# Optimization experiments

Measured on AMD Instinct MI355X. Metric: run time of the kernel, lower is better.

Reference implementation:

```python
import jax, jax.numpy as jnp
import numpy as np

BIG = 1e10  # sentinel for invalid pairwise distances


def get_xyz(depth, fx, fy, cx, cy):
    # depth: [B,1,H,W] -> xyz: [B,3,H,W] via pinhole unprojection
    B, _, H, W = depth.shape
    v = jnp.arange(H, dtype=depth.dtype)[:, None]   # rows
    u = jnp.arange(W, dtype=depth.dtype)[None, :]   # cols
    z = depth[:, 0]                                  # [B,H,W]
    x = (u - cx) / fx * z
    y = (v - cy) / fy * z
    return jnp.stack([x, y, z], axis=1)              # [B,3,H,W]


def _chamfer_item(p, g, vp, vg):
    # p,g: [N,3] point sets; vp,vg: [N] bool validity masks
    # squared pairwise distances via ||p||^2 + ||g||^2 - 2 p.g
    d = (jnp.sum(p * p, -1)[:, None] + jnp.sum(g * g, -1)[None, :]
         - 2.0 * (p @ g.T))                          # [N,N]
    d = jnp.maximum(d, 0.0)
    has_g = jnp.any(vg)
    has_p = jnp.any(vp)
    d1 = jnp.min(jnp.where(vg[None, :], d, BIG), axis=1)  # per pred point
    d2 = jnp.min(jnp.where(vp[:, None], d, BIG), axis=0)  # per gt point
    s1 = jnp.sum(jnp.where(vp & has_g, d1, 0.0))
    s2 = jnp.sum(jnp.where(vg & has_p, d2, 0.0))
    return s1 + s2


def reference(pred, gt_xyz, mask, fx, fy, cx, cy):
    B = pred.shape[0]
    pred_xyz = get_xyz(pred, fx, fy, cx, cy)             # [B,3,H,W]
    p = pred_xyz.reshape(B, 3, -1).transpose(0, 2, 1)    # [B,N,3]
    g = gt_xyz.reshape(B, 3, -1).transpose(0, 2, 1)      # [B,N,3]
    m = mask[:, 0].reshape(B, -1) > 0                    # [B,N]
    # ignore_zeros=True: drop points whose coordinate sum is exactly 0
    vp = m & (jnp.sum(p, -1) != 0)
    vg = m & (jnp.sum(g, -1) != 0)
    per_item = jax.vmap(_chamfer_item)(p, g, vp, vg)     # [B]
    return jnp.sum(per_item) / B


def setup_inputs() -> dict:
    key = jax.random.key(0)
    k1, k2, k3 = jax.random.split(key, 3)
    B, H, W = 2, 128, 128
    pred = jax.random.uniform(k1, (B, 1, H, W), dtype=jnp.float32) * 2.0 + 0.1
    gt_xyz = jax.random.normal(k2, (B, 3, H, W), dtype=jnp.float32)
    mask = jax.random.randint(k3, (B, 1, H, W), 0, 2, dtype=jnp.int32)
    fx = jnp.float32(525.0)
    fy = jnp.float32(525.0)
    cx = jnp.float32(64.0)
    cy = jnp.float32(64.0)
    return {"pred": pred, "gt_xyz": gt_xyz, "mask": mask,
            "fx": fx, "fy": fy, "cx": cx, "cy": cy}
```

## Files before the change

### kernel.cpp

```cpp
#include <hip/hip_runtime.h>

#define B_ITEMS 2
#define W_IMG   128
#define N_PTS   16384
#define QS      2
#define CH_GRID 2048
#define BIGF    3.4e38f

typedef float __attribute__((ext_vector_type(2))) f32x2;
typedef float __attribute__((ext_vector_type(4))) f32x4;

__global__ __launch_bounds__(256) void prep_kernel(
        const float* __restrict__ pred,
        const float* __restrict__ gt,
        const int*   __restrict__ mask,
        const float* fxp, const float* fyp,
        const float* cxp, const float* cyp,
        int*    __restrict__ cnt,
        float4* __restrict__ pR, float4* __restrict__ gR,
        float4* __restrict__ pT, float4* __restrict__ gT,
        float*  __restrict__ rmG,
        float*  __restrict__ out) {
    int s    = blockIdx.x >> 6;
    int b    = s & 1;
    int isG  = s >> 1;
    int tid  = threadIdx.x;
    int idx  = (blockIdx.x & 63) * 256 + tid;
    int lane = tid & 63, w = tid >> 6;

    if (blockIdx.x == 0 && tid == 0) out[0] = 0.0f;
    rmG[(blockIdx.x << 8) + tid] = BIGF;

    float x, y, z;
    if (!isG) {
        float fx = *fxp, fy = *fyp, cx = *cxp, cy = *cyp;
        float u = (float)(idx & (W_IMG - 1));
        float v = (float)(idx >> 7);
        z = pred[b * N_PTS + idx];
        x = (u - cx) / fx * z;
        y = (v - cy) / fy * z;
    } else {
        x = gt[(b * 3 + 0) * N_PTS + idx];
        y = gt[(b * 3 + 1) * N_PTS + idx];
        z = gt[(b * 3 + 2) * N_PTS + idx];
    }
    int  mv = mask[b * N_PTS + idx];
    bool ok = (mv > 0) && (((x + y) + z) != 0.0f);

    unsigned long long bal = __ballot(ok);
    int nw  = __popcll(bal);
    int pre = __popcll(bal & ((1ull << lane) - 1ull));

    __shared__ int wbase[4];
    __shared__ int blockbase;
    if (lane == 0) wbase[w] = nw;
    __syncthreads();
    if (tid == 0) {
        int s0 = 0;
#pragma unroll
        for (int i = 0; i < 4; ++i) { int t = wbase[i]; wbase[i] = s0; s0 += t; }
        blockbase = s0 ? atomicAdd(&cnt[s], s0) : 0;
    }
    __syncthreads();

    if (ok) {
        int pos = blockbase + wbase[w] + pre;
        float ps = fmaf(z, z, fmaf(y, y, x * x));
        float4* __restrict__ raw = (isG ? gR : pR) + b * N_PTS;
        float4* __restrict__ tf  = (isG ? gT : pT) + b * N_PTS;
        raw[pos] = make_float4(x, y, z, ps);
        tf[pos]  = make_float4(-2.0f * x, -2.0f * y, -2.0f * z, ps);
    }
}

__global__ __launch_bounds__(1024) void pad_kernel(
        const int* __restrict__ cnt,
        float4* __restrict__ pT, float4* __restrict__ gT) {
    int s = blockIdx.x;
    float4* arr = ((s >> 1) ? gT : pT) + (s & 1) * N_PTS;
    int n = cnt[s];
    int pos = n + threadIdx.x;
    if (pos < ((n + 1023) & ~1023))
        arr[pos] = make_float4(0.0f, 0.0f, 0.0f, BIGF);
}

#define VMCNT(n) asm volatile("s_waitcnt vmcnt(" #n ")" ::: "memory")

__device__ __forceinline__ void stage_tile(const float4* __restrict__ src,
                                           float4* lds_base, int w, int lane) {
    const float4* s0 = src + w * 128 + lane;
    __builtin_amdgcn_global_load_lds(
        (const __attribute__((address_space(1))) void*)(s0),
        (__attribute__((address_space(3))) void*)(lds_base + w * 128), 16, 0, 0);
    __builtin_amdgcn_global_load_lds(
        (const __attribute__((address_space(1))) void*)(s0 + 64),
        (__attribute__((address_space(3))) void*)(lds_base + w * 128 + 64), 16, 0, 0);
}

__global__ __launch_bounds__(256, 4) void chamfer_kernel(
        const int*    __restrict__ cnt,
        const float4* __restrict__ pR, const float4* __restrict__ gR,
        const float4* __restrict__ pT, const float4* __restrict__ gT,
        float* __restrict__ rmG) {
    int np0 = cnt[0], np1 = cnt[1], ng0 = cnt[2], ng1 = cnt[3];
    int naArr[4] = {np0, ng0, np1, ng1};
    int nbArr[4] = {ng0, np0, ng1, np1};
    const float4* Arow[4] = {pR, gR, pR + N_PTS, gR + N_PTS};
    const float4* Bcol[4] = {gT, pT, gT + N_PTS, pT + N_PTS};

    int units[4];
    int Utot = 0;
#pragma unroll
    for (int i = 0; i < 4; ++i) {
        units[i] = (naArr[i] > 0 && nbArr[i] > 0) ? (((naArr[i] + 63) >> 6) * QS) : 0;
        Utot += units[i];
    }

    int u = blockIdx.x;
    if (u >= Utot) return;
    int s = 0;
    while (u >= units[s]) { u -= units[s]; ++s; }
    int na = naArr[s], nb = nbArr[s];
    const float4* __restrict__ A  = Arow[s];
    const float4* __restrict__ Bp = Bcol[s];
    int q       = u & (QS - 1);
    int rowbase = (u >> 1) * 64;

    int nbPad  = (nb + 1023) & ~1023;
    int Lq     = nbPad >> 1;
    int cb0    = q * Lq;
    int ntiles = Lq >> 9;

    int tid  = threadIdx.x;
    int lane = tid & 63;
    int w    = tid >> 6;
    int tc   = tid & 31, tr = tid >> 5;

    f32x2 pxd[4], pyd[4], pzd[4];
    float rm[8];
#pragma unroll
    for (int a = 0; a < 4; ++a) {
        float4 v0 = A[rowbase + (2 * a) * 8 + tr];
        float4 v1 = A[rowbase + (2 * a + 1) * 8 + tr];
        pxd[a] = f32x2{v0.x, v1.x};
        pyd[a] = f32x2{v0.y, v1.y};
        pzd[a] = f32x2{v0.z, v1.z};
        rm[2 * a] = BIGF; rm[2 * a + 1] = BIGF;
    }

    __shared__ float4 sB[4][512];
    __shared__ float  smin[64];

    const float4* __restrict__ Bq = Bp + cb0;

    if (0 < ntiles) stage_tile(Bq, sB[0], w, lane);
    if (1 < ntiles) stage_tile(Bq + 512, sB[1], w, lane);
    if (2 < ntiles) stage_tile(Bq + 1024, sB[2], w, lane);

#define PKDIST(D, XY, ZW, a) { \
    asm("v_pk_fma_f32 %0, %1, %2, %3 op_sel:[0,0,1] op_sel_hi:[1,0,1]" \
        : "=v"(D) : "v"(pzd[a]), "v"(ZW), "v"(ZW)); \
    asm("v_pk_fma_f32 %0, %1, %2, %3 op_sel:[0,1,0] op_sel_hi:[1,1,1]" \
        : "=v"(D) : "v"(pyd[a]), "v"(XY), "v"(D)); \
    asm("v_pk_fma_f32 %0, %1, %2, %3 op_sel:[0,0,0] op_sel_hi:[1,0,1]" \
        : "=v"(D) : "v"(pxd[a]), "v"(XY), "v"(D)); }

#pragma unroll 1
    for (int t = 0; t < ntiles; ++t) {
        int rem = ntiles - 1 - t;
        if (rem >= 2)      { VMCNT(4); }
        else if (rem == 1) { VMCNT(2); }
        else               { VMCNT(0); }
        __builtin_amdgcn_s_barrier();
        __builtin_amdgcn_sched_barrier(0);
        if (t + 3 < ntiles)
            stage_tile(Bq + (t + 3) * 512, sB[(t + 3) & 3], w, lane);
        const f32x4* bufc = (const f32x4*)&sB[t & 3][tc];
#pragma unroll
        for (int cb = 0; cb < 16; cb += 2) {
            f32x4 c0 = bufc[cb * 32];
            f32x4 c1 = bufc[cb * 32 + 32];
            f32x2 c0xy = c0.xy, c0zw = c0.zw;
            f32x2 c1xy = c1.xy, c1zw = c1.zw;
#pragma unroll
            for (int a = 0; a < 4; ++a) {
                f32x2 d0, d1;
                PKDIST(d0, c0xy, c0zw, a)
                PKDIST(d1, c1xy, c1zw, a)
                rm[2 * a]     = fminf(fminf(rm[2 * a],     d0.x), d1.x);
                rm[2 * a + 1] = fminf(fminf(rm[2 * a + 1], d0.y), d1.y);
            }
        }
    }
#undef PKDIST

#pragma unroll
    for (int a = 0; a < 8; ++a) {
        float v = rm[a];
        v = fminf(v, __shfl_xor(v, 1, 64));
        v = fminf(v, __shfl_xor(v, 2, 64));
        v = fminf(v, __shfl_xor(v, 4, 64));
        v = fminf(v, __shfl_xor(v, 8, 64));
        v = fminf(v, __shfl_xor(v, 16, 64));
        rm[a] = v;
    }
    if (tc == 0) {
#pragma unroll
        for (int a = 0; a < 8; ++a) smin[a * 8 + tr] = rm[a];
    }
    __syncthreads();
    if (tid < 64) {
        int row = rowbase + tid;
        float v  = smin[tid];
        if (row < na) {
            float ps = A[row].w;
            float vr = fmaxf(v + ps, 0.0f);
            atomicMin((int*)&rmG[(s << 14) + row], __float_as_int(vr));
        }
    }
}

__global__ __launch_bounds__(256) void finish_kernel(
        const int*   __restrict__ cnt,
        const float* __restrict__ rmG,
        float*       __restrict__ out) {
    int gid = blockIdx.x * 256 + threadIdx.x;
    int s   = gid >> 14;
    int row = gid & (N_PTS - 1);
    int np0 = cnt[0], np1 = cnt[1], ng0 = cnt[2], ng1 = cnt[3];
    int naArr[4] = {np0, ng0, np1, ng1};
    int nbArr[4] = {ng0, np0, ng1, np1};
    float v = (row < naArr[s] && nbArr[s] > 0) ? rmG[gid] : 0.0f;
#pragma unroll
    for (int off = 32; off > 0; off >>= 1)
        v += __shfl_down(v, off, 64);
    __shared__ float wsum[4];
    if ((threadIdx.x & 63) == 0) wsum[threadIdx.x >> 6] = v;
    __syncthreads();
    if (threadIdx.x == 0) {
        float t = (wsum[0] + wsum[1]) + (wsum[2] + wsum[3]);
        atomicAdd(out, t * (1.0f / B_ITEMS));
    }
}

extern "C" void kernel_launch(void* const* d_in, const int* in_sizes, int n_in,
                              void* d_out, int out_size, void* d_ws, size_t ws_size,
                              hipStream_t stream) {
    const float* pred = (const float*)d_in[0];
    const float* gt   = (const float*)d_in[1];
    const int*   mask = (const int*)  d_in[2];
    const float* fx   = (const float*)d_in[3];
    const float* fy   = (const float*)d_in[4];
    const float* cx   = (const float*)d_in[5];
    const float* cy   = (const float*)d_in[6];
    float* out = (float*)d_out;

    char* ws = (char*)d_ws;
    size_t SEG = (size_t)B_ITEMS * N_PTS * 16;
    int*    cnt = (int*)ws;
    float4* pR  = (float4*)(ws + 256);
    float4* gR  = (float4*)(ws + 256 + SEG);
    float4* pT  = (float4*)(ws + 256 + 2 * SEG);
    float4* gT  = (float4*)(ws + 256 + 3 * SEG);
    float*  rmG = (float*) (ws + 256 + 4 * SEG);

    hipMemsetAsync(cnt, 0, 16, stream);

    prep_kernel<<<dim3(256), 256, 0, stream>>>(
        pred, gt, mask, fx, fy, cx, cy, cnt, pR, gR, pT, gT, rmG, out);

    pad_kernel<<<dim3(4), 1024, 0, stream>>>(cnt, pT, gT);

    chamfer_kernel<<<dim3(CH_GRID), 256, 0, stream>>>(
        cnt, pR, gR, pT, gT, rmG);

    finish_kernel<<<dim3(256), 256, 0, stream>>>(cnt, rmG, out);
}
```

Baseline: 102.6 us.

## Remap thread tiling so each wave owns 16 rows across all 512 columns

Changes the register tile from 8 rows x 16 columns per thread (32 column lanes by 8 row groups) to 16 rows x 8 columns per thread. Each wave now owns 16 contiguous query rows and its 64 lanes sweep the column tile. This doubles the work done per LDS load of a candidate point, cutting shared-memory read traffic per distance computed. In exchange it raises register pressure (24 packed coordinate registers plus 16 running minima) and adds one more shuffle stage to the final reduction.

```diff
diff --git a/kernel.cpp b/kernel.cpp
--- a/kernel.cpp
+++ b/kernel.cpp
@@ -134,18 +134,17 @@
     int tid  = threadIdx.x;
     int lane = tid & 63;
     int w    = tid >> 6;
-    int tc   = tid & 31, tr = tid >> 5;
-
-    f32x2 pxd[4], pyd[4], pzd[4];
-    float rm[8];
-#pragma unroll
-    for (int a = 0; a < 4; ++a) {
-        float4 v0 = A[rowbase + (2 * a) * 8 + tr];
-        float4 v1 = A[rowbase + (2 * a + 1) * 8 + tr];
+
+    f32x2 pxd[8], pyd[8], pzd[8];
+    float rmA[8], rmB[8];
+#pragma unroll
+    for (int a = 0; a < 8; ++a) {
+        float4 v0 = A[rowbase + w * 16 + 2 * a];
+        float4 v1 = A[rowbase + w * 16 + 2 * a + 1];
         pxd[a] = f32x2{v0.x, v1.x};
         pyd[a] = f32x2{v0.y, v1.y};
         pzd[a] = f32x2{v0.z, v1.z};
-        rm[2 * a] = BIGF; rm[2 * a + 1] = BIGF;
+        rmA[a] = BIGF; rmB[a] = BIGF;
     }
 
     __shared__ float4 sB[4][512];
@@ -175,20 +174,20 @@
         __builtin_amdgcn_sched_barrier(0);
         if (t + 3 < ntiles)
             stage_tile(Bq + (t + 3) * 512, sB[(t + 3) & 3], w, lane);
-        const f32x4* bufc = (const f32x4*)&sB[t & 3][tc];
-#pragma unroll
-        for (int cb = 0; cb < 16; cb += 2) {
-            f32x4 c0 = bufc[cb * 32];
-            f32x4 c1 = bufc[cb * 32 + 32];
+        const f32x4* bufc = (const f32x4*)&sB[t & 3][lane];
+#pragma unroll
+        for (int g = 0; g < 8; g += 2) {
+            f32x4 c0 = bufc[g * 64];
+            f32x4 c1 = bufc[g * 64 + 64];
             f32x2 c0xy = c0.xy, c0zw = c0.zw;
             f32x2 c1xy = c1.xy, c1zw = c1.zw;
 #pragma unroll
-            for (int a = 0; a < 4; ++a) {
+            for (int a = 0; a < 8; ++a) {
                 f32x2 d0, d1;
                 PKDIST(d0, c0xy, c0zw, a)
                 PKDIST(d1, c1xy, c1zw, a)
-                rm[2 * a]     = fminf(fminf(rm[2 * a],     d0.x), d1.x);
-                rm[2 * a + 1] = fminf(fminf(rm[2 * a + 1], d0.y), d1.y);
+                rmA[a] = fminf(fminf(rmA[a], d0.x), d1.x);
+                rmB[a] = fminf(fminf(rmB[a], d0.y), d1.y);
             }
         }
     }
@@ -196,17 +195,27 @@
 
 #pragma unroll
     for (int a = 0; a < 8; ++a) {
-        float v = rm[a];
-        v = fminf(v, __shfl_xor(v, 1, 64));
-        v = fminf(v, __shfl_xor(v, 2, 64));
-        v = fminf(v, __shfl_xor(v, 4, 64));
-        v = fminf(v, __shfl_xor(v, 8, 64));
-        v = fminf(v, __shfl_xor(v, 16, 64));
-        rm[a] = v;
-    }
-    if (tc == 0) {
-#pragma unroll
-        for (int a = 0; a < 8; ++a) smin[a * 8 + tr] = rm[a];
+        float vA = rmA[a], vB = rmB[a];
+        vA = fminf(vA, __shfl_xor(vA, 1, 64));
+        vB = fminf(vB, __shfl_xor(vB, 1, 64));
+        vA = fminf(vA, __shfl_xor(vA, 2, 64));
+        vB = fminf(vB, __shfl_xor(vB, 2, 64));
+        vA = fminf(vA, __shfl_xor(vA, 4, 64));
+        vB = fminf(vB, __shfl_xor(vB, 4, 64));
+        vA = fminf(vA, __shfl_xor(vA, 8, 64));
+        vB = fminf(vB, __shfl_xor(vB, 8, 64));
+        vA = fminf(vA, __shfl_xor(vA, 16, 64));
+        vB = fminf(vB, __shfl_xor(vB, 16, 64));
+        vA = fminf(vA, __shfl_xor(vA, 32, 64));
+        vB = fminf(vB, __shfl_xor(vB, 32, 64));
+        rmA[a] = vA; rmB[a] = vB;
+    }
+    if (lane == 0) {
+#pragma unroll
+        for (int a = 0; a < 8; ++a) {
+            smin[w * 16 + 2 * a]     = rmA[a];
+            smin[w * 16 + 2 * a + 1] = rmB[a];
+        }
     }
     __syncthreads();
     if (tid < 64) {
```

After: 102.0 us. No clear change (-0.5%).
